# Kernel tuning notes

Hardware: AMD Instinct MI355X
Metric: run time of the kernel (lower is better)

The kernel has to match this reference:

```python
import jax, jax.numpy as jnp
import numpy as np

NUM_HEADS = 16
NUM_KV_HEADS = 4
HEAD_DIM = 128
BASE_THETA = 10000.0


def _rope_cos_sin(seq_len, head_dim, dtype):
    # standard (ntk_alpha=1) rotate-half RoPE tables: [S, head_dim]
    inv_freq = 1.0 / (BASE_THETA ** (jnp.arange(0, head_dim, 2, dtype=jnp.float32) / head_dim))
    angles = jnp.arange(seq_len, dtype=jnp.float32)[:, None] * inv_freq[None, :]  # [S, D/2]
    cos = jnp.concatenate([jnp.cos(angles), jnp.cos(angles)], axis=-1).astype(dtype)
    sin = jnp.concatenate([jnp.sin(angles), jnp.sin(angles)], axis=-1).astype(dtype)
    return cos, sin


def _rotate_half(t):
    half = t.shape[-1] // 2
    return jnp.concatenate([-t[..., half:], t[..., :half]], axis=-1)


def setup_inputs() -> dict:
    key = jax.random.key(0)
    ks = jax.random.split(key, 5)
    B, S, E = 2, 2048, 2048
    KV = NUM_KV_HEADS * HEAD_DIM  # 512
    scale = 0.02
    return {
        "x": jax.random.normal(ks[0], (B, S, E), dtype=jnp.float32),
        "Wq": jax.random.normal(ks[1], (E, E), dtype=jnp.float32) * scale,
        "Wk": jax.random.normal(ks[2], (E, KV), dtype=jnp.float32) * scale,
        "Wv": jax.random.normal(ks[3], (E, KV), dtype=jnp.float32) * scale,
        "Wo": jax.random.normal(ks[4], (E, E), dtype=jnp.float32) * scale,
    }


def reference(x, Wq, Wk, Wv, Wo):
    B, S, E = x.shape
    n_rep = NUM_HEADS // NUM_KV_HEADS
    scale = 1.0 / jnp.sqrt(jnp.float32(HEAD_DIM))

    # QKV projections (bias=False)
    q = (x @ Wq).reshape(B, S, NUM_HEADS, HEAD_DIM)
    k = (x @ Wk).reshape(B, S, NUM_KV_HEADS, HEAD_DIM)
    v = (x @ Wv).reshape(B, S, NUM_KV_HEADS, HEAD_DIM)

    # dynamic RoPE on q, k
    cos, sin = _rope_cos_sin(S, HEAD_DIM, x.dtype)
    cos = cos[None, :, None, :]
    sin = sin[None, :, None, :]
    q = q * cos + _rotate_half(q) * sin
    k = k * cos + _rotate_half(k) * sin

    # GQA: repeat kv heads to match query heads
    k = jnp.repeat(k, n_rep, axis=2)
    v = jnp.repeat(v, n_rep, axis=2)

    # [B, H, S, D]
    q = q.transpose(0, 2, 1, 3)
    k = k.transpose(0, 2, 1, 3)
    v = v.transpose(0, 2, 1, 3)

    # causal mask (window_size=0 -> standard causal, additive float mask)
    i = jnp.arange(S)[:, None]
    j = jnp.arange(S)[None, :]
    neg = jnp.finfo(jnp.float32).min
    causal = jnp.where(j > i, neg, 0.0).astype(jnp.float32)  # [S, S]

    scores = jnp.einsum("bhqd,bhkd->bhqk", q, k) * scale
    scores = scores + causal[None, None, :, :]
    weights = jax.nn.softmax(scores.astype(jnp.float32), axis=-1)
    attn = jnp.einsum("bhqk,bhkd->bhqd", weights.astype(v.dtype), v)

    attn = attn.transpose(0, 2, 1, 3).reshape(B, S, E)
    return attn @ Wo
```

## Files before the change

### kernel.cpp

```cpp
#include <hip/hip_runtime.h>
#include <math.h>


typedef __attribute__((ext_vector_type(8))) short short8;
typedef __attribute__((ext_vector_type(4))) float f32x4;

typedef const __attribute__((address_space(1))) void* gvp;
typedef __attribute__((address_space(3))) void* svp;

__device__ __forceinline__ void async16(const void* g, void* l) {
  __builtin_amdgcn_global_load_lds((gvp)g, (svp)l, 16, 0, 0);
}
__device__ __forceinline__ void wait_vm0() { asm volatile("s_waitcnt vmcnt(0)" ::: "memory"); }
__device__ __forceinline__ void barrier_raw() { asm volatile("s_barrier" ::: "memory"); }

__device__ __forceinline__ unsigned short f2b(float f) {
  unsigned int u = __builtin_bit_cast(unsigned int, f);
  u += 0x7fffu + ((u >> 16) & 1u);
  return (unsigned short)(u >> 16);
}
__device__ __forceinline__ float b2f(unsigned short h) {
  unsigned int u = ((unsigned int)h) << 16;
  return __builtin_bit_cast(float, u);
}

__global__ __launch_bounds__(256) void convx(const float* __restrict__ x,
                                             unsigned short* __restrict__ xb) {
  int i = blockIdx.x * 256 + threadIdx.x;
  const float4* p = (const float4*)x + (size_t)i * 2;
  float4 a = p[0], b4 = p[1];
  union { short8 v; unsigned short u[8]; } o;
  o.u[0] = f2b(a.x);  o.u[1] = f2b(a.y);  o.u[2] = f2b(a.z);  o.u[3] = f2b(a.w);
  o.u[4] = f2b(b4.x); o.u[5] = f2b(b4.y); o.u[6] = f2b(b4.z); o.u[7] = f2b(b4.w);
  ((short8*)xb)[i] = o.v;
}

__global__ __launch_bounds__(256) void wconv_all(const float* __restrict__ Wq,
                                                 const float* __restrict__ Wk,
                                                 const float* __restrict__ Wv,
                                                 const float* __restrict__ Wo,
                                                 unsigned short* __restrict__ WqkvT,
                                                 unsigned short* __restrict__ WoT) {
  __shared__ float t[32][33];
  int idx = blockIdx.x;
  const float* W; unsigned short* WT; int N, tx, ty;
  const int K = 2048;
  if (idx < 4096)      { W = Wq; WT = WqkvT;                         N = 2048; idx -= 0;    tx = idx & 63; ty = idx >> 6; }
  else if (idx < 5120) { W = Wk; WT = WqkvT + (size_t)2048 * 2048;   N = 512;  idx -= 4096; tx = idx & 15; ty = idx >> 4; }
  else if (idx < 6144) { W = Wv; WT = WqkvT + (size_t)2560 * 2048;   N = 512;  idx -= 5120; tx = idx & 15; ty = idx >> 4; }
  else                 { W = Wo; WT = WoT;                           N = 2048; idx -= 6144; tx = idx & 63; ty = idx >> 6; }
  int c = threadIdx.x & 31, r0 = threadIdx.x >> 5;
  int k0 = ty * 32, n0 = tx * 32;
#pragma unroll
  for (int r = r0; r < 32; r += 8) t[r][c] = W[(size_t)(k0 + r) * N + n0 + c];
  __syncthreads();
#pragma unroll
  for (int r = r0; r < 32; r += 8) WT[(size_t)(n0 + r) * K + k0 + c] = f2b(t[c][r]);
}

__global__ __launch_bounds__(256) void gemm_bt(const unsigned short* __restrict__ A,
                                               const unsigned short* __restrict__ BT,
                                               void* __restrict__ Cout,
                                               int M, int N, int K, int out_bf16) {
  const int n0 = blockIdx.x * 128;
  const int m0 = blockIdx.y * 128;
  const int tid = threadIdx.x;
  const int w = tid >> 6, lane = tid & 63, l15 = lane & 15, quad = lane >> 4;
  const int wm = w >> 1, wn = w & 1;

  __shared__ __align__(16) unsigned short As[2][128 * 64];
  __shared__ __align__(16) unsigned short Bs[2][128 * 64];

  f32x4 acc[4][4];
#pragma unroll
  for (int mi = 0; mi < 4; mi++)
#pragma unroll
    for (int ni = 0; ni < 4; ni++) acc[mi][ni] = (f32x4){0.f, 0.f, 0.f, 0.f};

  const int rl = lane >> 3;
  const int cl = lane & 7;
  const unsigned short* Ab = A + (size_t)m0 * K;
  const unsigned short* Bb = BT + (size_t)n0 * K;

#pragma unroll
  for (int i = 0; i < 4; i++) {
    int row = w * 32 + i * 8 + rl;
    int gc = cl ^ (row & 7);
    async16(Ab + (size_t)row * K + gc * 8, &As[0][(w * 32 + i * 8) * 64]);
    async16(Bb + (size_t)row * K + gc * 8, &Bs[0][(w * 32 + i * 8) * 64]);
  }

  const int nIter = K >> 6;
  for (int j = 0; j < nIter; j++) {
    wait_vm0();
    barrier_raw();
    const int cur = j & 1;

    if (j + 1 < nIter) {
      int kb = (j + 1) * 64;
#pragma unroll
      for (int i = 0; i < 4; i++) {
        int row = w * 32 + i * 8 + rl;
        int gc = cl ^ (row & 7);
        async16(Ab + (size_t)row * K + kb + gc * 8, &As[cur ^ 1][(w * 32 + i * 8) * 64]);
        async16(Bb + (size_t)row * K + kb + gc * 8, &Bs[cur ^ 1][(w * 32 + i * 8) * 64]);
      }
    }

    const unsigned short* as = &As[cur][0];
    const unsigned short* bs = &Bs[cur][0];
#pragma unroll
    for (int kk = 0; kk < 2; kk++) {
      short8 af[4], bfv[4];
#pragma unroll
      for (int mi = 0; mi < 4; mi++) {
        int row = wm * 64 + mi * 16 + l15;
        af[mi] = *(const short8*)&as[row * 64 + (((kk * 4 + quad) ^ (row & 7)) * 8)];
      }
#pragma unroll
      for (int ni = 0; ni < 4; ni++) {
        int row = wn * 64 + ni * 16 + l15;
        bfv[ni] = *(const short8*)&bs[row * 64 + (((kk * 4 + quad) ^ (row & 7)) * 8)];
      }
#pragma unroll
      for (int mi = 0; mi < 4; mi++)
#pragma unroll
        for (int ni = 0; ni < 4; ni++)
          acc[mi][ni] = __builtin_amdgcn_mfma_f32_16x16x32_bf16(af[mi], bfv[ni],
                                                                acc[mi][ni], 0, 0, 0);
    }
  }

  if (out_bf16) {
    unsigned short* C = (unsigned short*)Cout;
#pragma unroll
    for (int mi = 0; mi < 4; mi++)
#pragma unroll
      for (int ni = 0; ni < 4; ni++)
#pragma unroll
        for (int r = 0; r < 4; r++) {
          int row = m0 + wm * 64 + mi * 16 + quad * 4 + r;
          int col = n0 + wn * 64 + ni * 16 + l15;
          C[(size_t)row * N + col] = f2b(acc[mi][ni][r]);
        }
  } else {
    float* C = (float*)Cout;
#pragma unroll
    for (int mi = 0; mi < 4; mi++)
#pragma unroll
      for (int ni = 0; ni < 4; ni++)
#pragma unroll
        for (int r = 0; r < 4; r++) {
          int row = m0 + wm * 64 + mi * 16 + quad * 4 + r;
          int col = n0 + wn * 64 + ni * 16 + l15;
          C[(size_t)row * N + col] = acc[mi][ni][r];
        }
  }
}

#define SC_TOT 0.12753785056274918f
__global__ __launch_bounds__(256) void rope_kernel(const unsigned short* __restrict__ qkv,
                                                   unsigned short* __restrict__ Q,
                                                   unsigned short* __restrict__ Kd) {
  int b = blockIdx.z, hh = blockIdx.y;
  int tid = threadIdx.x;
  int d = tid & 63, sl = tid >> 6;
  int s = blockIdx.x * 4 + sl;
  const unsigned short* src = qkv + ((size_t)(b * 2048 + s)) * 3072 + hh * 128;
  float lo = b2f(src[d]), hi = b2f(src[d + 64]);
  float invf = exp2f(-0.20762050593046f * (float)d);
  float ang = (float)s * invf;
  float sn, cs;
  sincosf(ang, &sn, &cs);
  float nlo = lo * cs - hi * sn;
  float nhi = hi * cs + lo * sn;
  unsigned short* dst;
  if (hh < 16) {
    nlo *= SC_TOT; nhi *= SC_TOT;
    dst = Q + ((size_t)((b * 16 + hh) * 2048 + s)) * 128;
  } else {
    dst = Kd + ((size_t)((b * 4 + (hh - 16)) * 2048 + s)) * 128;
  }
  dst[d] = f2b(nlo);
  dst[d + 64] = f2b(nhi);
}

__global__ __launch_bounds__(256) void vtrans(const unsigned short* __restrict__ qkv,
                                              unsigned short* __restrict__ Vt) {
  int bkv = blockIdx.z;
  int b = bkv >> 2, kv = bkv & 3;
  int s0 = blockIdx.x * 64, d0 = blockIdx.y * 64;
  __shared__ unsigned short t[64][65];
  int c = threadIdx.x & 63, r0 = threadIdx.x >> 6;
  const unsigned short* src = qkv + ((size_t)(b * 2048 + s0)) * 3072 + 2560 + kv * 128 + d0;
#pragma unroll
  for (int r = r0; r < 64; r += 4) t[r][c] = src[(size_t)r * 3072 + c];
  __syncthreads();
  unsigned short* dst = Vt + ((size_t)bkv * 128 + d0) * 2048 + s0;
#pragma unroll
  for (int r = r0; r < 64; r += 4) dst[(size_t)r * 2048 + c] = t[c][r];
}

#define FIXED_M 12.0f
__global__ __launch_bounds__(256) void flash2(const unsigned short* __restrict__ Q,
                                              const unsigned short* __restrict__ Kc,
                                              const unsigned short* __restrict__ Vt,
                                              unsigned short* __restrict__ attn) {
  const int pair = blockIdx.x;
  const int h = blockIdx.y;
  const int b = blockIdx.z;
  const int kvh = h >> 2;
  const int tid = threadIdx.x;
  const int w = tid >> 6, lane = tid & 63, l15 = lane & 15, quad = lane >> 4;

  __shared__ __align__(16) unsigned short kbuf[2][64 * 128];
  __shared__ __align__(16) unsigned short vbuf[2][128 * 64];
  __shared__ __align__(16) unsigned short pbuf[4][16 * 64];

  const unsigned short* Qb = Q  + ((size_t)(b * 16 + h)) * 2048 * 128;
  const unsigned short* Kb = Kc + ((size_t)(b * 4 + kvh)) * 2048 * 128;
  const unsigned short* Vb = Vt + ((size_t)(b * 4 + kvh)) * 128 * 2048;
  unsigned short* pb = &pbuf[w][0];

  for (int t = 0; t < 2; t++) {
    const int qt = (t == 0) ? pair : (31 - pair);
    const int q0 = qt * 64;
    const int nT = qt + 1;

    short8 qf[4];
    {
      const unsigned short* qp = Qb + (size_t)(q0 + w * 16 + l15) * 128 + quad * 8;
#pragma unroll
      for (int kk = 0; kk < 4; kk++) qf[kk] = *(const short8*)(qp + kk * 32);
    }

    float l_i[4];
    f32x4 o[8];
#pragma unroll
    for (int r = 0; r < 4; r++) l_i[r] = 0.f;
#pragma unroll
    for (int nn = 0; nn < 8; nn++) o[nn] = (f32x4){0.f, 0.f, 0.f, 0.f};

    barrier_raw();

#pragma unroll
    for (int k = 0; k < 4; k++) {
      int m = w * 4 + k;
      int rl = m * 4 + (lane >> 4);
      int c8 = (lane & 15) ^ (rl & 7);
      async16(Kb + (size_t)rl * 128 + c8 * 8, &kbuf[0][m * 512]);
    }
#pragma unroll
    for (int k = 0; k < 4; k++) {
      int m = w * 4 + k;
      int d = m * 8 + (lane >> 3);
      int c3 = (lane & 7) ^ (d & 7);
      async16(Vb + (size_t)d * 2048 + c3 * 8, &vbuf[0][m * 512]);
    }

    for (int j = 0; j < nT; j++) {
      wait_vm0();
      barrier_raw();
      const int cur = j & 1;

      if (j + 1 < nT) {
        int j1 = (j + 1) * 64;
#pragma unroll
        for (int k = 0; k < 4; k++) {
          int m = w * 4 + k;
          int rl = m * 4 + (lane >> 4);
          int c8 = (lane & 15) ^ (rl & 7);
          async16(Kb + (size_t)(j1 + rl) * 128 + c8 * 8, &kbuf[cur ^ 1][m * 512]);
        }
#pragma unroll
        for (int k = 0; k < 4; k++) {
          int m = w * 4 + k;
          int d = m * 8 + (lane >> 3);
          int c3 = (lane & 7) ^ (d & 7);
          async16(Vb + (size_t)d * 2048 + (j + 1) * 64 + c3 * 8, &vbuf[cur ^ 1][m * 512]);
        }
      }

      const unsigned short* kb = &kbuf[cur][0];
      const unsigned short* vb = &vbuf[cur][0];

      f32x4 s4[4];
#pragma unroll
      for (int nn = 0; nn < 4; nn++) {
        f32x4 a = (f32x4){0.f, 0.f, 0.f, 0.f};
        int row = nn * 16 + l15;
#pragma unroll
        for (int kk = 0; kk < 4; kk++) {
          short8 bfr = *(const short8*)&kb[row * 128 + (((kk * 4 + quad) ^ (row & 7)) * 8)];
          a = __builtin_amdgcn_mfma_f32_16x16x32_bf16(qf[kk], bfr, a, 0, 0, 0);
        }
        s4[nn] = a;
      }

      const bool diag = (j * 64 == q0);
      const int myrow = w * 16 + quad * 4;
#pragma unroll
      for (int nn = 0; nn < 4; nn++) {
        int col = nn * 16 + l15;
#pragma unroll
        for (int r = 0; r < 4; r++) {
          float p = exp2f(s4[nn][r] - FIXED_M);
          if (diag && (col > myrow + r)) p = 0.f;
          l_i[r] += p;
          int prow = quad * 4 + r;
          pb[prow * 64 + ((nn * 2 + (l15 >> 3)) ^ (prow & 7)) * 8 + (l15 & 7)] = f2b(p);
        }
      }

#pragma unroll
      for (int ks = 0; ks < 2; ks++) {
        short8 af = *(const short8*)&pb[l15 * 64 + (((ks * 4 + quad) ^ (l15 & 7)) * 8)];
#pragma unroll
        for (int nn = 0; nn < 8; nn++) {
          int d = nn * 16 + l15;
          short8 bfr = *(const short8*)&vb[d * 64 + (((ks * 4 + quad) ^ (d & 7)) * 8)];
          o[nn] = __builtin_amdgcn_mfma_f32_16x16x32_bf16(af, bfr, o[nn], 0, 0, 0);
        }
      }
    }

#pragma unroll
    for (int r = 0; r < 4; r++) {
#pragma unroll
      for (int off = 1; off < 16; off <<= 1) l_i[r] += __shfl_xor(l_i[r], off, 64);
    }
    float inv[4];
#pragma unroll
    for (int r = 0; r < 4; r++) inv[r] = 1.f / l_i[r];
    unsigned short* ap = attn + ((size_t)(b * 2048 + q0 + w * 16)) * 2048 + h * 128;
#pragma unroll
    for (int nn = 0; nn < 8; nn++)
#pragma unroll
      for (int r = 0; r < 4; r++)
        ap[(size_t)(quad * 4 + r) * 2048 + nn * 16 + l15] = f2b(o[nn][r] * inv[r]);
  }
}

extern "C" void kernel_launch(void* const* d_in, const int* in_sizes, int n_in,
                              void* d_out, int out_size, void* d_ws, size_t ws_size,
                              hipStream_t stream) {
  const float* x  = (const float*)d_in[0];
  const float* Wq = (const float*)d_in[1];
  const float* Wk = (const float*)d_in[2];
  const float* Wv = (const float*)d_in[3];
  const float* Wo = (const float*)d_in[4];
  float* out = (float*)d_out;

  char* ws = (char*)d_ws;
  unsigned short* xb    = (unsigned short*)(ws);
  unsigned short* WqkvT = (unsigned short*)(ws + 16777216);
  unsigned short* WoT   = (unsigned short*)(ws + 29360128);
  unsigned short* qkv   = (unsigned short*)(ws + 37748736);
  unsigned short* Qm    = (unsigned short*)(ws + 62914560);
  unsigned short* Km    = (unsigned short*)(ws + 79691776);
  unsigned short* Vtm   = (unsigned short*)(ws + 83886080);
  unsigned short* attn  = xb;

  convx<<<4096, 256, 0, stream>>>(x, xb);
  wconv_all<<<10240, 256, 0, stream>>>(Wq, Wk, Wv, Wo, WqkvT, WoT);

  gemm_bt<<<dim3(24, 32), 256, 0, stream>>>(xb, WqkvT, qkv, 4096, 3072, 2048, 1);

  rope_kernel<<<dim3(512, 20, 2), 256, 0, stream>>>(qkv, Qm, Km);
  vtrans<<<dim3(32, 2, 8), 256, 0, stream>>>(qkv, Vtm);

  flash2<<<dim3(16, 16, 2), 256, 0, stream>>>(Qm, Km, Vtm, attn);

  gemm_bt<<<dim3(16, 32), 256, 0, stream>>>(attn, WoT, out, 4096, 2048, 2048, 0);
}
```

Baseline: 311.8 us.

## Restructure flash attention into one q-tile per block with 32-wide KV tiles

The attention kernel drops the paired q-tile scheme. Each block now handles one q-tile, heaviest tiles first, and streams 32-key KV tiles through smaller double-buffered LDS. Warps skip KV tiles that lie entirely above their causal rows, and row sums are computed with an MFMA against a ones vector instead of scalar adds plus shuffles. RoPE switches to hardware sin/cos on range-reduced revolutions. The changes aim at better occupancy, finer causal skipping and less VALU work, at the cost of more barrier iterations per block and slightly lower precision in the RoPE sin/cos.

```diff
diff --git a/kernel.cpp b/kernel.cpp
--- a/kernel.cpp
+++ b/kernel.cpp
@@ -168,10 +168,11 @@
   int s = blockIdx.x * 4 + sl;
   const unsigned short* src = qkv + ((size_t)(b * 2048 + s)) * 3072 + hh * 128;
   float lo = b2f(src[d]), hi = b2f(src[d + 64]);
-  float invf = exp2f(-0.20762050593046f * (float)d);
-  float ang = (float)s * invf;
-  float sn, cs;
-  sincosf(ang, &sn, &cs);
+  float invf_rev = exp2f(-0.20762050593046f * (float)d) * 0.15915494309189535f;
+  float rev = (float)s * invf_rev;
+  float fr = rev - floorf(rev);
+  float sn = __builtin_amdgcn_sinf(fr);
+  float cs = __builtin_amdgcn_cosf(fr);
   float nlo = lo * cs - hi * sn;
   float nhi = hi * cs + lo * sn;
   unsigned short* dst;
@@ -202,143 +203,139 @@
 }
 
 #define FIXED_M 12.0f
-__global__ __launch_bounds__(256) void flash2(const unsigned short* __restrict__ Q,
-                                              const unsigned short* __restrict__ Kc,
-                                              const unsigned short* __restrict__ Vt,
-                                              unsigned short* __restrict__ attn) {
-  const int pair = blockIdx.x;
+__global__ __launch_bounds__(256, 4) void flash3(const unsigned short* __restrict__ Q,
+                                                 const unsigned short* __restrict__ Kc,
+                                                 const unsigned short* __restrict__ Vt,
+                                                 unsigned short* __restrict__ attn) {
+  const int qt = 31 - blockIdx.x;
   const int h = blockIdx.y;
   const int b = blockIdx.z;
   const int kvh = h >> 2;
   const int tid = threadIdx.x;
   const int w = tid >> 6, lane = tid & 63, l15 = lane & 15, quad = lane >> 4;
 
-  __shared__ __align__(16) unsigned short kbuf[2][64 * 128];
-  __shared__ __align__(16) unsigned short vbuf[2][128 * 64];
-  __shared__ __align__(16) unsigned short pbuf[4][16 * 64];
+  __shared__ __align__(16) unsigned short kbuf[2][32 * 128];
+  __shared__ __align__(16) unsigned short vbuf[2][128 * 32];
+  __shared__ __align__(16) unsigned short pbuf[4][16 * 32];
 
   const unsigned short* Qb = Q  + ((size_t)(b * 16 + h)) * 2048 * 128;
   const unsigned short* Kb = Kc + ((size_t)(b * 4 + kvh)) * 2048 * 128;
   const unsigned short* Vb = Vt + ((size_t)(b * 4 + kvh)) * 128 * 2048;
   unsigned short* pb = &pbuf[w][0];
 
-  for (int t = 0; t < 2; t++) {
-    const int qt = (t == 0) ? pair : (31 - pair);
-    const int q0 = qt * 64;
-    const int nT = qt + 1;
-
-    short8 qf[4];
+  const int q0 = qt * 64;
+  const int nT = 2 * qt + 2;
+  const int rowbase = q0 + w * 16;
+
+  short8 qf[4];
+  {
+    const unsigned short* qp = Qb + (size_t)(rowbase + l15) * 128 + quad * 8;
+#pragma unroll
+    for (int kk = 0; kk < 4; kk++) qf[kk] = *(const short8*)(qp + kk * 32);
+  }
+
+  short8 ones;
+  {
+    union { short8 v; unsigned short u[8]; } t;
+#pragma unroll
+    for (int i = 0; i < 8; i++) t.u[i] = 0x3F80;
+    ones = t.v;
+  }
+
+  f32x4 o[8], lacc;
+#pragma unroll
+  for (int nn = 0; nn < 8; nn++) o[nn] = (f32x4){0.f, 0.f, 0.f, 0.f};
+  lacc = (f32x4){0.f, 0.f, 0.f, 0.f};
+
+#pragma unroll
+  for (int k = 0; k < 2; k++) {
+    int m = w * 2 + k;
     {
-      const unsigned short* qp = Qb + (size_t)(q0 + w * 16 + l15) * 128 + quad * 8;
-#pragma unroll
-      for (int kk = 0; kk < 4; kk++) qf[kk] = *(const short8*)(qp + kk * 32);
-    }
-
-    float l_i[4];
-    f32x4 o[8];
-#pragma unroll
-    for (int r = 0; r < 4; r++) l_i[r] = 0.f;
-#pragma unroll
-    for (int nn = 0; nn < 8; nn++) o[nn] = (f32x4){0.f, 0.f, 0.f, 0.f};
-
+      int row = m * 4 + (lane >> 4);
+      int gc = (lane & 15) ^ (row & 7);
+      async16(Kb + (size_t)row * 128 + gc * 8, &kbuf[0][m * 512]);
+    }
+    {
+      int d = m * 16 + (lane >> 2);
+      int gc = (lane & 3) ^ ((d >> 1) & 3);
+      async16(Vb + (size_t)d * 2048 + gc * 8, &vbuf[0][m * 512]);
+    }
+  }
+
+  for (int j = 0; j < nT; j++) {
+    wait_vm0();
     barrier_raw();
-
-#pragma unroll
-    for (int k = 0; k < 4; k++) {
-      int m = w * 4 + k;
-      int rl = m * 4 + (lane >> 4);
-      int c8 = (lane & 15) ^ (rl & 7);
-      async16(Kb + (size_t)rl * 128 + c8 * 8, &kbuf[0][m * 512]);
-    }
-#pragma unroll
-    for (int k = 0; k < 4; k++) {
-      int m = w * 4 + k;
-      int d = m * 8 + (lane >> 3);
-      int c3 = (lane & 7) ^ (d & 7);
-      async16(Vb + (size_t)d * 2048 + c3 * 8, &vbuf[0][m * 512]);
-    }
-
-    for (int j = 0; j < nT; j++) {
-      wait_vm0();
-      barrier_raw();
-      const int cur = j & 1;
-
-      if (j + 1 < nT) {
-        int j1 = (j + 1) * 64;
-#pragma unroll
-        for (int k = 0; k < 4; k++) {
-          int m = w * 4 + k;
-          int rl = m * 4 + (lane >> 4);
-          int c8 = (lane & 15) ^ (rl & 7);
-          async16(Kb + (size_t)(j1 + rl) * 128 + c8 * 8, &kbuf[cur ^ 1][m * 512]);
+    const int cur = j & 1;
+
+    if (j + 1 < nT) {
+      int k1 = (j + 1) * 32;
+#pragma unroll
+      for (int k = 0; k < 2; k++) {
+        int m = w * 2 + k;
+        {
+          int row = m * 4 + (lane >> 4);
+          int gc = (lane & 15) ^ (row & 7);
+          async16(Kb + (size_t)(k1 + row) * 128 + gc * 8, &kbuf[cur ^ 1][m * 512]);
         }
-#pragma unroll
-        for (int k = 0; k < 4; k++) {
-          int m = w * 4 + k;
-          int d = m * 8 + (lane >> 3);
-          int c3 = (lane & 7) ^ (d & 7);
-          async16(Vb + (size_t)d * 2048 + (j + 1) * 64 + c3 * 8, &vbuf[cur ^ 1][m * 512]);
+        {
+          int d = m * 16 + (lane >> 2);
+          int gc = (lane & 3) ^ ((d >> 1) & 3);
+          async16(Vb + (size_t)d * 2048 + k1 + gc * 8, &vbuf[cur ^ 1][m * 512]);
         }
       }
-
-      const unsigned short* kb = &kbuf[cur][0];
-      const unsigned short* vb = &vbuf[cur][0];
-
-      f32x4 s4[4];
-#pragma unroll
-      for (int nn = 0; nn < 4; nn++) {
-        f32x4 a = (f32x4){0.f, 0.f, 0.f, 0.f};
-        int row = nn * 16 + l15;
-#pragma unroll
-        for (int kk = 0; kk < 4; kk++) {
-          short8 bfr = *(const short8*)&kb[row * 128 + (((kk * 4 + quad) ^ (row & 7)) * 8)];
-          a = __builtin_amdgcn_mfma_f32_16x16x32_bf16(qf[kk], bfr, a, 0, 0, 0);
-        }
-        s4[nn] = a;
-      }
-
-      const bool diag = (j * 64 == q0);
-      const int myrow = w * 16 + quad * 4;
-#pragma unroll
-      for (int nn = 0; nn < 4; nn++) {
-        int col = nn * 16 + l15;
-#pragma unroll
-        for (int r = 0; r < 4; r++) {
-          float p = exp2f(s4[nn][r] - FIXED_M);
-          if (diag && (col > myrow + r)) p = 0.f;
-          l_i[r] += p;
-          int prow = quad * 4 + r;
-          pb[prow * 64 + ((nn * 2 + (l15 >> 3)) ^ (prow & 7)) * 8 + (l15 & 7)] = f2b(p);
-        }
-      }
-
-#pragma unroll
-      for (int ks = 0; ks < 2; ks++) {
-        short8 af = *(const short8*)&pb[l15 * 64 + (((ks * 4 + quad) ^ (l15 & 7)) * 8)];
-#pragma unroll
-        for (int nn = 0; nn < 8; nn++) {
-          int d = nn * 16 + l15;
-          short8 bfr = *(const short8*)&vb[d * 64 + (((ks * 4 + quad) ^ (d & 7)) * 8)];
-          o[nn] = __builtin_amdgcn_mfma_f32_16x16x32_bf16(af, bfr, o[nn], 0, 0, 0);
-        }
-      }
-    }
-
-#pragma unroll
-    for (int r = 0; r < 4; r++) {
-#pragma unroll
-      for (int off = 1; off < 16; off <<= 1) l_i[r] += __shfl_xor(l_i[r], off, 64);
-    }
-    float inv[4];
-#pragma unroll
-    for (int r = 0; r < 4; r++) inv[r] = 1.f / l_i[r];
-    unsigned short* ap = attn + ((size_t)(b * 2048 + q0 + w * 16)) * 2048 + h * 128;
-#pragma unroll
-    for (int nn = 0; nn < 8; nn++)
-#pragma unroll
-      for (int r = 0; r < 4; r++)
-        ap[(size_t)(quad * 4 + r) * 2048 + nn * 16 + l15] = f2b(o[nn][r] * inv[r]);
-  }
+    }
+
+    if (32 * j > rowbase + 15) continue;
+
+    const unsigned short* kb = &kbuf[cur][0];
+    const unsigned short* vb = &vbuf[cur][0];
+
+    f32x4 s4[2];
+#pragma unroll
+    for (int nn = 0; nn < 2; nn++) {
+      f32x4 a = (f32x4){0.f, 0.f, 0.f, 0.f};
+      int row = nn * 16 + l15;
+#pragma unroll
+      for (int kk = 0; kk < 4; kk++) {
+        short8 bfr = *(const short8*)&kb[row * 128 + (((kk * 4 + quad) ^ (row & 7)) * 8)];
+        a = __builtin_amdgcn_mfma_f32_16x16x32_bf16(qf[kk], bfr, a, 0, 0, 0);
+      }
+      s4[nn] = a;
+    }
+
+    const bool needmask = (32 * j + 31 > rowbase);
+#pragma unroll
+    for (int nn = 0; nn < 2; nn++) {
+      int col = 32 * j + nn * 16 + l15;
+#pragma unroll
+      for (int r = 0; r < 4; r++) {
+        float p = exp2f(s4[nn][r] - FIXED_M);
+        if (needmask && (col > rowbase + quad * 4 + r)) p = 0.f;
+        int prow = quad * 4 + r;
+        int c = nn * 2 + (l15 >> 3);
+        pb[prow * 32 + ((c ^ quad) * 8) + (l15 & 7)] = f2b(p);
+      }
+    }
+
+    short8 af = *(const short8*)&pb[l15 * 32 + ((quad ^ (l15 >> 2)) * 8)];
+    lacc = __builtin_amdgcn_mfma_f32_16x16x32_bf16(af, ones, lacc, 0, 0, 0);
+#pragma unroll
+    for (int nn = 0; nn < 8; nn++) {
+      int d = nn * 16 + l15;
+      short8 bfr = *(const short8*)&vb[d * 32 + ((quad ^ ((d >> 1) & 3)) * 8)];
+      o[nn] = __builtin_amdgcn_mfma_f32_16x16x32_bf16(af, bfr, o[nn], 0, 0, 0);
+    }
+  }
+
+  float inv[4];
+#pragma unroll
+  for (int r = 0; r < 4; r++) inv[r] = 1.f / lacc[r];
+  unsigned short* ap = attn + ((size_t)(b * 2048 + rowbase)) * 2048 + h * 128;
+#pragma unroll
+  for (int nn = 0; nn < 8; nn++)
+#pragma unroll
+    for (int r = 0; r < 4; r++)
+      ap[(size_t)(quad * 4 + r) * 2048 + nn * 16 + l15] = f2b(o[nn][r] * inv[r]);
 }
 
 extern "C" void kernel_launch(void* const* d_in, const int* in_sizes, int n_in,
@@ -369,7 +366,7 @@
   rope_kernel<<<dim3(512, 20, 2), 256, 0, stream>>>(qkv, Qm, Km);
   vtrans<<<dim3(32, 2, 8), 256, 0, stream>>>(qkv, Vtm);
 
-  flash2<<<dim3(16, 16, 2), 256, 0, stream>>>(Qm, Km, Vtm, attn);
+  flash3<<<dim3(32, 16, 2), 256, 0, stream>>>(Qm, Km, Vtm, attn);
 
   gemm_bt<<<dim3(16, 32), 256, 0, stream>>>(attn, WoT, out, 4096, 2048, 2048, 0);
 }
```

Result: slower. 353.8 us (+13.4%).
